# Kernel tuning notes

Hardware: AMD Instinct MI355X
Metric: run time of the kernel (lower is better)

The kernel has to match this reference:

```python
import jax, jax.numpy as jnp
import numpy as np
import math
from math import ceil

# --- static configuration (matches init_kwargs / input_specs) ---
T, H, W = 10, 45, 80            # native 720p latent video grid
NUM_WIN = (2, 5, 5)             # num_windows passed to make_720Pwindows_bysize
D_MODEL = 512
HEADS = 4
HEAD_DIM = 128
ROPE_DIMS = (32, 48, 48)        # 3D RoPE split of head_dim over (t, h, w)
THETA = 10000.0
TXT_LEN = 64
N_VID = T * H * W


def _make_windows():
    """Replicates make_720Pwindows_bysize slicing; returns gather/scatter index tables."""
    t, h, w = T, H, W
    rnt, rnh, rnw = NUM_WIN
    scale = math.sqrt(45 * 80 / (h * w))
    rh, rw = round(h * scale), round(w * scale)
    wh, ww = ceil(rh / rnh), ceil(rw / rnw)
    wt = ceil(min(t, 30) / rnt)
    nt, nh, nw = ceil(t / wt), ceil(h / wh), ceil(w / ww)
    lin = np.arange(t * h * w).reshape(t, h, w)
    wins = []
    for iw in range(nw):
        for ih in range(nh):
            for it in range(nt):
                ts = slice(it * wt, min((it + 1) * wt, t))
                hs = slice(ih * wh, min((ih + 1) * wh, h))
                ws = slice(iw * ww, min((iw + 1) * ww, w))
                blk = lin[ts, hs, ws].reshape(-1)
                if blk.size:
                    wins.append(blk)
    assert len({x.size for x in wins}) == 1, 'chosen dims give uniform windows'
    idx = np.stack(wins)                      # [n_win, win_size] gather index
    src = np.argsort(idx.reshape(-1))         # inverse permutation (un-window)
    return idx, src

WIN_IDX_NP, SRC_IDX_NP = _make_windows()
N_WIN, WIN_SIZE = WIN_IDX_NP.shape


def _rope_tables():
    """3D RoPE cos/sin per vid token: head_dim split over (t,h,w) axes, interleaved pairs."""
    tt = np.broadcast_to(np.arange(T)[:, None, None], (T, H, W)).reshape(-1)
    hh = np.broadcast_to(np.arange(H)[None, :, None], (T, H, W)).reshape(-1)
    ww = np.broadcast_to(np.arange(W)[None, None, :], (T, H, W)).reshape(-1)
    cos_l, sin_l = [], []
    for pos, d in zip((tt, hh, ww), ROPE_DIMS):
        inv = 1.0 / (THETA ** (np.arange(0, d, 2, dtype=np.float64) / d))
        ang = pos[:, None].astype(np.float64) * inv[None, :]
        ang = np.repeat(ang, 2, axis=-1)
        cos_l.append(np.cos(ang))
        sin_l.append(np.sin(ang))
    cos = np.concatenate(cos_l, -1).astype(np.float32)
    sin = np.concatenate(sin_l, -1).astype(np.float32)
    return jnp.asarray(cos), jnp.asarray(sin)  # each [N_VID, HEAD_DIM]

ROPE_COS, ROPE_SIN = _rope_tables()


def _rotate_half(x):
    # '... (d r) -> ... d r' with r=2, then (-x2, x1) re-interleaved
    xr = x.reshape(x.shape[:-1] + (-1, 2))
    x1, x2 = xr[..., 0], xr[..., 1]
    return jnp.stack((-x2, x1), axis=-1).reshape(x.shape)


def _apply_rope(x, cos, sin):
    # x: [N, heads, D]; cos/sin: [N, D]
    return x * cos[:, None, :] + _rotate_half(x) * sin[:, None, :]


def setup_inputs() -> dict:
    key = jax.random.key(0)
    ks = jax.random.split(key, 6)
    s = 1.0 / math.sqrt(D_MODEL)
    return {
        'vid': jax.random.normal(ks[0], (N_VID, D_MODEL), jnp.float32),
        'txt': jax.random.normal(ks[1], (TXT_LEN, D_MODEL), jnp.float32),
        'w_qkv_vid': jax.random.normal(ks[2], (D_MODEL, 3 * D_MODEL), jnp.float32) * s,
        'w_qkv_txt': jax.random.normal(ks[3], (D_MODEL, 3 * D_MODEL), jnp.float32) * s,
        'w_out_vid': jax.random.normal(ks[4], (D_MODEL, D_MODEL), jnp.float32) * s,
        'w_out_txt': jax.random.normal(ks[5], (D_MODEL, D_MODEL), jnp.float32) * s,
    }


def reference(vid, txt, w_qkv_vid, w_qkv_txt, w_out_vid, w_out_txt):
    win_idx = jnp.asarray(WIN_IDX_NP)
    src_idx = jnp.asarray(SRC_IDX_NP)
    # per-modality QKV projection (MMModule: separate vid/txt weights)
    qkv_v = (vid @ w_qkv_vid).reshape(N_VID, 3, HEADS, HEAD_DIM)
    qv, kv, vv = qkv_v[:, 0], qkv_v[:, 1], qkv_v[:, 2]
    qv = _apply_rope(qv, ROPE_COS, ROPE_SIN)   # 3D RoPE on video q/k only
    kv = _apply_rope(kv, ROPE_COS, ROPE_SIN)
    qkv_t = (txt @ w_qkv_txt).reshape(TXT_LEN, 3, HEADS, HEAD_DIM)
    qt, kt, vt = qkv_t[:, 0], qkv_t[:, 1], qkv_t[:, 2]

    def win_cat(xv, xt):
        xw = xv[win_idx]
        xtb = jnp.broadcast_to(xt[None], (N_WIN,) + xt.shape)    # txt repeated per window
        return jnp.concatenate([xw, xtb], axis=1)                # [n_win, S, H, D]

    q, k, v = win_cat(qv, qt), win_cat(kv, kt), win_cat(vv, vt)
    scale = 1.0 / math.sqrt(HEAD_DIM)
    scores = jnp.einsum('wqhd,wkhd->whqk', q, k) * scale         # [n_win, H, S, S]
    probs = jax.nn.softmax(scores, axis=-1)
    out = jnp.einsum('whqk,wkhd->wqhd', probs, v)                # [n_win, S, H, D]
    # un-window vid tokens (inverse permutation), mean-coalesce txt over windows
    out_v = out[:, :WIN_SIZE].reshape(N_WIN * WIN_SIZE, D_MODEL)[src_idx]
    out_t = out[:, WIN_SIZE:].mean(axis=0).reshape(TXT_LEN, D_MODEL)
    return jnp.concatenate([out_v @ w_out_vid, out_t @ w_out_txt], axis=0)
```

## Files before the change

kernel.cpp:

```cpp
#include <hip/hip_runtime.h>
#include <hip/hip_bf16.h>


typedef unsigned short u16;
typedef unsigned int   u32;
typedef float v4f __attribute__((ext_vector_type(4)));
typedef short v8s __attribute__((ext_vector_type(8)));

#define N_VID    36000
#define MPAD     36096
#define DM       512
#define NW       50
#define WSZ      720
#define SEQ      784
#define SP       832
#define QK_SCALE 0.08838834764831845f
#define L2THETA  13.287712379549449f

union U8 { uint4 u; u16 s[8]; };

__device__ __forceinline__ u16 f2b(float f) {
  u32 u = __builtin_bit_cast(u32, f);
  u32 r = (u + 0x7FFFu + ((u >> 16) & 1u)) >> 16;
  return (u16)r;
}
__device__ __forceinline__ float b2f(u16 h) {
  u32 u = ((u32)h) << 16;
  return __builtin_bit_cast(float, u);
}

__device__ __forceinline__ void gload_lds16(const void* g, void* l) {
  __builtin_amdgcn_global_load_lds(
      (const __attribute__((address_space(1))) void*)g,
      (__attribute__((address_space(3))) void*)l,
      16, 0, 0);
}

__global__ __launch_bounds__(256) void k_convert(const float* __restrict__ vid,
                                                 const float* __restrict__ txt,
                                                 u16* __restrict__ vid_b,
                                                 u16* __restrict__ txt_b) {
  int id  = blockIdx.x * 256 + threadIdx.x;
  int row = id >> 6, oct = id & 63;
  U8 o;
  if (row < MPAD) {
    if (row < N_VID) {
      const float* s = vid + (size_t)row * DM + oct * 8;
      float4 a = *(const float4*)s, b = *(const float4*)(s + 4);
      o.s[0]=f2b(a.x); o.s[1]=f2b(a.y); o.s[2]=f2b(a.z); o.s[3]=f2b(a.w);
      o.s[4]=f2b(b.x); o.s[5]=f2b(b.y); o.s[6]=f2b(b.z); o.s[7]=f2b(b.w);
    } else { o.u = make_uint4(0,0,0,0); }
    *(uint4*)&vid_b[(size_t)row * DM + oct * 8] = o.u;
  } else {
    int tr = row - MPAD;
    if (tr >= 128) return;
    if (tr < 64) {
      const float* s = txt + (size_t)tr * DM + oct * 8;
      float4 a = *(const float4*)s, b = *(const float4*)(s + 4);
      o.s[0]=f2b(a.x); o.s[1]=f2b(a.y); o.s[2]=f2b(a.z); o.s[3]=f2b(a.w);
      o.s[4]=f2b(b.x); o.s[5]=f2b(b.y); o.s[6]=f2b(b.z); o.s[7]=f2b(b.w);
    } else { o.u = make_uint4(0,0,0,0); }
    *(uint4*)&txt_b[(size_t)tr * DM + oct * 8] = o.u;
  }
}

__global__ __launch_bounds__(256) void k_transw(const float* __restrict__ wqv,
                                                const float* __restrict__ wqt,
                                                const float* __restrict__ wov,
                                                u16* __restrict__ o0,
                                                u16* __restrict__ o1,
                                                u16* __restrict__ o2) {
  __shared__ u16 lt[64 * 72];
  int b = blockIdx.x, t = threadIdx.x;
  const float* src; u16* dst; int N; int tb;
  if (b < 192)      { src = wqv; dst = o0; N = 1536; tb = b; }
  else if (b < 384) { src = wqt; dst = o1; N = 1536; tb = b - 192; }
  else              { src = wov; dst = o2; N = 512;  tb = b - 384; }
  int kt = tb & 7, nt = tb >> 3;
  int k0 = kt * 64, n0 = nt * 64;
#pragma unroll
  for (int pass = 0; pass < 16; ++pass) {
    int kl = pass * 4 + (t >> 6), nl = t & 63;
    float v = src[(size_t)(k0 + kl) * N + n0 + nl];
    lt[nl * 72 + kl] = f2b(v);
  }
  __syncthreads();
#pragma unroll
  for (int pass = 0; pass < 2; ++pass) {
    int slot = pass * 256 + t;
    int nr = slot >> 3, ko = slot & 7;
    U8 o;
#pragma unroll
    for (int j = 0; j < 8; ++j) o.s[j] = lt[nr * 72 + ko * 8 + j];
    *(uint4*)&dst[(size_t)(n0 + nr) * 512 + k0 + ko * 8] = o.u;
  }
}

template <int F32OUT>
__global__ __launch_bounds__(256) void k_gemm(const u16* __restrict__ A,
                                              const u16* __restrict__ Bt,
                                              void* __restrict__ Cout,
                                              int M, int N, int K, int Mstore) {
  __shared__ u16 lA[128 * 32];
  __shared__ u16 lB[128 * 32];
  int t = threadIdx.x, wv = t >> 6, L = t & 63;
  int m0 = blockIdx.x * 128, n0 = blockIdx.y * 128;
  int wm = wv & 1, wn = wv >> 1;
  v4f acc[4][4] = {};
  const int kiters = K >> 5;
  const u16* ga = A + (size_t)(m0 + wv * 32 + (L >> 2)) * K + (L & 3) * 8;
  const u16* gb = Bt + (size_t)(n0 + wv * 32 + (L >> 2)) * K + (L & 3) * 8;
  u16* la = lA + (wv * 32) * 32;
  u16* lb = lB + (wv * 32) * 32;
  for (int kt = 0; kt < kiters; ++kt) {
    __syncthreads();
    gload_lds16(ga,                 la);
    gload_lds16(ga + (size_t)16 * K, la + 16 * 32);
    gload_lds16(gb,                 lb);
    gload_lds16(gb + (size_t)16 * K, lb + 16 * 32);
    ga += 32; gb += 32;
    __syncthreads();
    v8s af[4], bf[4];
#pragma unroll
    for (int i = 0; i < 4; ++i) {
      af[i] = *(const v8s*)&lA[(wm * 64 + i * 16 + (L & 15)) * 32 + (L >> 4) * 8];
      bf[i] = *(const v8s*)&lB[(wn * 64 + i * 16 + (L & 15)) * 32 + (L >> 4) * 8];
    }
#pragma unroll
    for (int i = 0; i < 4; ++i)
#pragma unroll
      for (int j = 0; j < 4; ++j)
        acc[i][j] = __builtin_amdgcn_mfma_f32_16x16x32_bf16(af[i], bf[j], acc[i][j], 0, 0, 0);
  }
#pragma unroll
  for (int i = 0; i < 4; ++i) {
#pragma unroll
    for (int r = 0; r < 4; ++r) {
      int row = m0 + wm * 64 + i * 16 + (L >> 4) * 4 + r;
      if (row < Mstore) {
#pragma unroll
        for (int j = 0; j < 4; ++j) {
          int col = n0 + wn * 64 + j * 16 + (L & 15);
          if (F32OUT) ((float*)Cout)[(size_t)row * N + col] = acc[i][j][r];
          else        ((u16*)Cout)[(size_t)row * N + col] = f2b(acc[i][j][r]);
        }
      }
    }
  }
}

__global__ __launch_bounds__(256) void k_ropegather(const u16* __restrict__ qkv,
                                                    u16* __restrict__ Q,
                                                    u16* __restrict__ K,
                                                    u16* __restrict__ Vt) {
  __shared__ u16 lv[512 * 18];
  int t = threadIdx.x;
  int pt = blockIdx.x, w = blockIdx.y;
  int p_local = t >> 4;
  int p = pt * 16 + p_local;
  int iw = w / 10; int r10 = w - iw * 10; int ih = r10 >> 1; int it = r10 & 1;
  int dt = p / 144; int rem = p - dt * 144; int dh = rem >> 4; int dw = rem & 15;
  int tt = it * 5 + dt, hh = ih * 9 + dh, wx = iw * 16 + dw;
  int n = tt * 3600 + hh * 80 + wx;
  const size_t qrow = (size_t)n * 1536;
#pragma unroll
  for (int it2 = 0; it2 < 12; ++it2) {
    int oct = it2 * 16 + (t & 15);
    int col = oct * 8;
    U8 x; x.u = *(const uint4*)&qkv[qrow + col];
    if (col < 1024) {
      int cc = col & 511; int h = cc >> 7; int ch = cc & 127;
      int pos, i0; float dinv;
      if (ch < 32)      { pos = tt; i0 = ch >> 1;        dinv = 1.f / 32.f; }
      else if (ch < 80) { pos = hh; i0 = (ch - 32) >> 1; dinv = 1.f / 48.f; }
      else              { pos = wx; i0 = (ch - 80) >> 1; dinv = 1.f / 48.f; }
      bool isQ = col < 512;
      float sc = isQ ? QK_SCALE : 1.0f;
      U8 o;
#pragma unroll
      for (int pr = 0; pr < 4; ++pr) {
        float inv = exp2f(-2.f * (float)(i0 + pr) * dinv * L2THETA);
        float ang = (float)pos * inv;
        float s, c; __sincosf(ang, &s, &c);
        float x0 = b2f(x.s[2 * pr]), x1 = b2f(x.s[2 * pr + 1]);
        o.s[2 * pr]     = f2b((x0 * c - x1 * s) * sc);
        o.s[2 * pr + 1] = f2b((x1 * c + x0 * s) * sc);
      }
      u16* dst = isQ ? Q : K;
      *(uint4*)&dst[(((size_t)w * 4 + h) * SP + p) * 128 + ch] = o.u;
    } else {
      int cv = col - 1024;
#pragma unroll
      for (int j = 0; j < 8; ++j) lv[(cv + j) * 18 + p_local] = x.s[j];
    }
  }
  __syncthreads();
#pragma unroll
  for (int it3 = 0; it3 < 4; ++it3) {
    int slot = it3 * 256 + t; int cv = slot >> 1; int half = slot & 1;
    U8 o;
#pragma unroll
    for (int j = 0; j < 8; ++j) o.s[j] = lv[cv * 18 + half * 8 + j];
    int h = cv >> 7, ch = cv & 127;
    *(uint4*)&Vt[(((size_t)w * 4 + h) * 128 + ch) * SP + pt * 16 + half * 8] = o.u;
  }
}

__global__ __launch_bounds__(256) void k_txtfill(const u16* __restrict__ qkvt,
                                                 u16* __restrict__ Q,
                                                 u16* __restrict__ K,
                                                 u16* __restrict__ Vt) {
  int id = blockIdx.x * 256 + threadIdx.x;
  if (blockIdx.x < 800) {
    int c8 = id & 15, i = (id >> 4) & 63, wh = id >> 10;
    int h = wh & 3; int ch = c8 * 8;
    U8 q, k;
    q.u = *(const uint4*)&qkvt[(size_t)i * 1536 + h * 128 + ch];
    k.u = *(const uint4*)&qkvt[(size_t)i * 1536 + 512 + h * 128 + ch];
#pragma unroll
    for (int j = 0; j < 8; ++j) q.s[j] = f2b(b2f(q.s[j]) * QK_SCALE);
    int p = WSZ + i;
    size_t base = ((size_t)wh * SP + p) * 128 + ch;
    *(uint4*)&Q[base] = q.u;
    *(uint4*)&K[base] = k.u;
  } else {
    int id2 = id - 800 * 256;
    if (id2 >= 25600) return;
    int ch = id2 & 127; int wh = id2 >> 7; int h = wh & 3;
    u16 vals[64];
#pragma unroll
    for (int i = 0; i < 64; ++i)
      vals[i] = qkvt[(size_t)i * 1536 + 1024 + h * 128 + ch];
    size_t rb = ((size_t)wh * 128 + ch) * SP + WSZ;
#pragma unroll
    for (int j = 0; j < 8; ++j) {
      U8 o;
#pragma unroll
      for (int m = 0; m < 8; ++m) o.s[m] = vals[j * 8 + m];
      *(uint4*)&Vt[rb + j * 8] = o.u;
    }
  }
}

__global__ __launch_bounds__(256, 3) void k_attn(const u16* __restrict__ Q,
                                                 const u16* __restrict__ Kb,
                                                 const u16* __restrict__ Vt,
                                                 u16* __restrict__ outr,
                                                 float* __restrict__ txt_acc) {
  __shared__ u16 lK[4 * 64 * 32];
  __shared__ u16 lV[2 * 128 * 32];
  __shared__ u16 lP[4][32 * 72];
  int t = threadIdx.x, wv = t >> 6, L = t & 63;
  int qt = blockIdx.x, h = blockIdx.y, w = blockIdx.z;
  size_t whq = ((size_t)(w * 4 + h)) * SP * 128;
  int q0 = qt * 128 + wv * 32;
  if (q0 > 800) q0 = 800;
  int colL = L & 15;
  v8s qf[2][4];
#pragma unroll
  for (int s = 0; s < 2; ++s) {
    const u16* qp = Q + whq + (size_t)(q0 + s * 16 + colL) * 128 + (L >> 4) * 8;
#pragma unroll
    for (int kc = 0; kc < 4; ++kc) qf[s][kc] = *(const v8s*)(qp + kc * 32);
  }
  float li[2][4] = {};
  v4f O[2][8] = {};

  for (int kt = 0; kt < 13; ++kt) {
    __syncthreads();
#pragma unroll
    for (int pass = 0; pass < 4; ++pass) {
      int cr = wv * 64 + pass * 16 + (L >> 2);
      int kc = cr >> 6, row = cr & 63;
      gload_lds16(Kb + whq + (size_t)(kt * 64 + row) * 128 + kc * 32 + (L & 3) * 8,
                  (u16*)lK + (size_t)(wv * 64 + pass * 16) * 32);
      int kc2 = cr >> 7, ch = cr & 127;
      gload_lds16(Vt + whq + (size_t)ch * SP + kt * 64 + kc2 * 32 + (L & 3) * 8,
                  (u16*)lV + (size_t)(wv * 64 + pass * 16) * 32);
    }
    __syncthreads();

    v4f S[2][4] = {};
#pragma unroll
    for (int kc = 0; kc < 4; ++kc) {
#pragma unroll
      for (int nb = 0; nb < 4; ++nb) {
        v8s b = *(const v8s*)&lK[(kc * 64 + nb * 16 + colL) * 32 + (L >> 4) * 8];
        S[0][nb] = __builtin_amdgcn_mfma_f32_16x16x32_bf16(qf[0][kc], b, S[0][nb], 0, 0, 0);
        S[1][nb] = __builtin_amdgcn_mfma_f32_16x16x32_bf16(qf[1][kc], b, S[1][nb], 0, 0, 0);
      }
    }

#pragma unroll
    for (int s = 0; s < 2; ++s) {
#pragma unroll
      for (int nb = 0; nb < 4; ++nb) {
        bool valid = (kt * 64 + nb * 16 + colL) < SEQ;
#pragma unroll
        for (int r = 0; r < 4; ++r) {
          float e = valid ? __expf(S[s][nb][r]) : 0.f;
          li[s][r] += e;
          lP[wv][(s * 16 + (L >> 4) * 4 + r) * 72 + nb * 16 + colL] = f2b(e);
        }
      }
    }

#pragma unroll
    for (int kc2 = 0; kc2 < 2; ++kc2) {
      v8s pa0 = *(const v8s*)&lP[wv][(colL) * 72 + kc2 * 32 + (L >> 4) * 8];
      v8s pa1 = *(const v8s*)&lP[wv][(16 + colL) * 72 + kc2 * 32 + (L >> 4) * 8];
#pragma unroll
      for (int nbo = 0; nbo < 8; ++nbo) {
        v8s vb = *(const v8s*)&lV[(kc2 * 128 + nbo * 16 + colL) * 32 + (L >> 4) * 8];
        O[0][nbo] = __builtin_amdgcn_mfma_f32_16x16x32_bf16(pa0, vb, O[0][nbo], 0, 0, 0);
        O[1][nbo] = __builtin_amdgcn_mfma_f32_16x16x32_bf16(pa1, vb, O[1][nbo], 0, 0, 0);
      }
    }
  }

#pragma unroll
  for (int s = 0; s < 2; ++s)
#pragma unroll
    for (int r = 0; r < 4; ++r) {
      float v = li[s][r];
#pragma unroll
      for (int msk = 1; msk < 16; msk <<= 1) v += __shfl_xor(v, msk);
      li[s][r] = 1.f / v;
    }

  int iw = w / 10; int r10 = w - iw * 10; int ih = r10 >> 1; int it = r10 & 1;
#pragma unroll
  for (int s = 0; s < 2; ++s) {
#pragma unroll
    for (int r = 0; r < 4; ++r) {
      int p = q0 + s * 16 + (L >> 4) * 4 + r;
      float linv = li[s][r];
      if (p < WSZ) {
        int dt = p / 144; int rem = p - dt * 144; int dh = rem >> 4; int dw = rem & 15;
        int n = (it * 5 + dt) * 3600 + (ih * 9 + dh) * 80 + iw * 16 + dw;
        size_t rowbase = (size_t)n * DM + h * 128 + colL;
#pragma unroll
        for (int nbo = 0; nbo < 8; ++nbo)
          outr[rowbase + nbo * 16] = f2b(O[s][nbo][r] * linv);
      } else if (p < SEQ) {
        size_t rb = (size_t)(p - WSZ) * DM + h * 128 + colL;
#pragma unroll
        for (int nbo = 0; nbo < 8; ++nbo)
          atomicAdd(&txt_acc[rb + nbo * 16], O[s][nbo][r] * linv * 0.02f);
      }
    }
  }
}

__global__ __launch_bounds__(256) void k_txtout(const float* __restrict__ acc,
                                                const float* __restrict__ wo,
                                                float* __restrict__ ob) {
  int r = blockIdx.x, t = threadIdx.x;
  float s0 = 0.f, s1 = 0.f;
  for (int k = 0; k < 512; ++k) {
    float a = acc[r * 512 + k];
    s0 = fmaf(a, wo[k * 512 + t], s0);
    s1 = fmaf(a, wo[k * 512 + t + 256], s1);
  }
  ob[(size_t)r * 512 + t] = s0;
  ob[(size_t)r * 512 + t + 256] = s1;
}

extern "C" void kernel_launch(void* const* d_in, const int* in_sizes, int n_in,
                              void* d_out, int out_size, void* d_ws, size_t ws_size,
                              hipStream_t stream) {
  const float* vid       = (const float*)d_in[0];
  const float* txt       = (const float*)d_in[1];
  const float* w_qkv_vid = (const float*)d_in[2];
  const float* w_qkv_txt = (const float*)d_in[3];
  const float* w_out_vid = (const float*)d_in[4];
  const float* w_out_txt = (const float*)d_in[5];
  float* out = (float*)d_out;
  char* ws = (char*)d_ws;

  size_t off = 0;
  u16* vid_b   = (u16*)(ws + off); off += (size_t)MPAD * DM * 2;
  u16* txt_b   = (u16*)(ws + off); off += 128 * DM * 2;
  u16* wt_qv   = (u16*)(ws + off); off += 1536 * 512 * 2;
  u16* wt_qt   = (u16*)(ws + off); off += 1536 * 512 * 2;
  u16* wt_ov   = (u16*)(ws + off); off += 512 * 512 * 2;
  u16* qkv_v   = (u16*)(ws + off); off += (size_t)MPAD * 1536 * 2;
  u16* qkv_t   = (u16*)(ws + off); off += 128 * 1536 * 2;
  u16* Qb      = (u16*)(ws + off); off += (size_t)NW * 4 * SP * 128 * 2;
  u16* Kb      = (u16*)(ws + off); off += (size_t)NW * 4 * SP * 128 * 2;
  u16* Vtb     = (u16*)(ws + off); off += (size_t)NW * 4 * 128 * SP * 2;
  float* tacc  = (float*)(ws + off); off += 64 * 512 * 4;
  u16* out_rows = vid_b;

  hipMemsetAsync(tacc, 0, 64 * 512 * 4, stream);

  k_convert<<<9056, 256, 0, stream>>>(vid, txt, vid_b, txt_b);
  k_transw<<<448, 256, 0, stream>>>(w_qkv_vid, w_qkv_txt, w_out_vid, wt_qv, wt_qt, wt_ov);

  k_gemm<0><<<dim3(282, 12), 256, 0, stream>>>(vid_b, wt_qv, qkv_v, MPAD, 1536, 512, MPAD);
  k_gemm<0><<<dim3(1, 12), 256, 0, stream>>>(txt_b, wt_qt, qkv_t, 128, 1536, 512, 128);

  k_ropegather<<<dim3(45, 50), 256, 0, stream>>>(qkv_v, Qb, Kb, Vtb);
  k_txtfill<<<900, 256, 0, stream>>>(qkv_t, Qb, Kb, Vtb);

  k_attn<<<dim3(7, 4, 50), 256, 0, stream>>>(Qb, Kb, Vtb, out_rows, tacc);

  k_gemm<1><<<dim3(282, 4), 256, 0, stream>>>(out_rows, wt_ov, out, MPAD, 512, 512, N_VID);
  k_txtout<<<64, 256, 0, stream>>>(tacc, w_out_txt, out + (size_t)N_VID * DM);
}
```

Measured before the change: 517.2 us.

## Compute transposed scores so softmax probabilities feed PV MFMA from registers

The attention kernel now computes S^T = K·Q^T, which puts each query's probabilities in the MFMA register layout needed as the B operand of the PV product. The LDS round trip through the per-wave lP buffer is removed, and the row-sum reduction shrinks to two cross-lane shuffles. Blocks are remapped onto a 1D grid so that all query tiles of one window-head pair land on the same XCD, aiming for better L2 reuse of K and V. Output stores are widened to 8-byte packed writes, and the launch-bounds occupancy hint is dropped, which may change register allocation.

```diff
diff --git a/kernel.cpp b/kernel.cpp
--- a/kernel.cpp
+++ b/kernel.cpp
@@ -6,6 +6,7 @@
 typedef unsigned int   u32;
 typedef float v4f __attribute__((ext_vector_type(4)));
 typedef short v8s __attribute__((ext_vector_type(8)));
+typedef short v4s __attribute__((ext_vector_type(4)));
 
 #define N_VID    36000
 #define MPAD     36096
@@ -27,6 +28,10 @@
 __device__ __forceinline__ float b2f(u16 h) {
   u32 u = ((u32)h) << 16;
   return __builtin_bit_cast(float, u);
+}
+__device__ __forceinline__ u32 pkhi(float lo, float hi) {
+  return __builtin_amdgcn_perm(__builtin_bit_cast(u32, hi),
+                               __builtin_bit_cast(u32, lo), 0x07060302u);
 }
 
 __device__ __forceinline__ void gload_lds16(const void* g, void* l) {
@@ -242,28 +247,31 @@
   }
 }
 
-__global__ __launch_bounds__(256, 3) void k_attn(const u16* __restrict__ Q,
-                                                 const u16* __restrict__ Kb,
-                                                 const u16* __restrict__ Vt,
-                                                 u16* __restrict__ outr,
-                                                 float* __restrict__ txt_acc) {
+__global__ __launch_bounds__(256) void k_attn(const u16* __restrict__ Q,
+                                              const u16* __restrict__ Kb,
+                                              const u16* __restrict__ Vt,
+                                              u16* __restrict__ outr,
+                                              float* __restrict__ txt_acc) {
   __shared__ u16 lK[4 * 64 * 32];
   __shared__ u16 lV[2 * 128 * 32];
-  __shared__ u16 lP[4][32 * 72];
   int t = threadIdx.x, wv = t >> 6, L = t & 63;
-  int qt = blockIdx.x, h = blockIdx.y, w = blockIdx.z;
-  size_t whq = ((size_t)(w * 4 + h)) * SP * 128;
+  int id = blockIdx.x;
+  int xcd = id & 7, sidx = id >> 3;
+  int whg = sidx / 7;  int qt = sidx - whg * 7;
+  int wh = whg * 8 + xcd;
+  int w = wh >> 2, h = wh & 3;
+  size_t whq = ((size_t)wh) * SP * 128;
   int q0 = qt * 128 + wv * 32;
   if (q0 > 800) q0 = 800;
-  int colL = L & 15;
+  int colL = L & 15, quad = L >> 4;
   v8s qf[2][4];
 #pragma unroll
   for (int s = 0; s < 2; ++s) {
-    const u16* qp = Q + whq + (size_t)(q0 + s * 16 + colL) * 128 + (L >> 4) * 8;
+    const u16* qp = Q + whq + (size_t)(q0 + s * 16 + colL) * 128 + quad * 8;
 #pragma unroll
     for (int kc = 0; kc < 4; ++kc) qf[s][kc] = *(const v8s*)(qp + kc * 32);
   }
-  float li[2][4] = {};
+  float li[2] = {0.f, 0.f};
   v4f O[2][8] = {};
 
   for (int kt = 0; kt < 13; ++kt) {
@@ -280,74 +288,86 @@
     }
     __syncthreads();
 
-    v4f S[2][4] = {};
+    v4f ST[2][4] = {};
 #pragma unroll
     for (int kc = 0; kc < 4; ++kc) {
 #pragma unroll
-      for (int nb = 0; nb < 4; ++nb) {
-        v8s b = *(const v8s*)&lK[(kc * 64 + nb * 16 + colL) * 32 + (L >> 4) * 8];
-        S[0][nb] = __builtin_amdgcn_mfma_f32_16x16x32_bf16(qf[0][kc], b, S[0][nb], 0, 0, 0);
-        S[1][nb] = __builtin_amdgcn_mfma_f32_16x16x32_bf16(qf[1][kc], b, S[1][nb], 0, 0, 0);
-      }
-    }
-
+      for (int nbk = 0; nbk < 4; ++nbk) {
+        v8s kf = *(const v8s*)&lK[(kc * 64 + nbk * 16 + colL) * 32 + quad * 8];
+        ST[0][nbk] = __builtin_amdgcn_mfma_f32_16x16x32_bf16(kf, qf[0][kc], ST[0][nbk], 0, 0, 0);
+        ST[1][nbk] = __builtin_amdgcn_mfma_f32_16x16x32_bf16(kf, qf[1][kc], ST[1][nbk], 0, 0, 0);
+      }
+    }
+
+    union { v8s v; u32 wd[4]; } Bf[2][2];
 #pragma unroll
     for (int s = 0; s < 2; ++s) {
 #pragma unroll
-      for (int nb = 0; nb < 4; ++nb) {
-        bool valid = (kt * 64 + nb * 16 + colL) < SEQ;
-#pragma unroll
-        for (int r = 0; r < 4; ++r) {
-          float e = valid ? __expf(S[s][nb][r]) : 0.f;
-          li[s][r] += e;
-          lP[wv][(s * 16 + (L >> 4) * 4 + r) * 72 + nb * 16 + colL] = f2b(e);
+      for (int nbk = 0; nbk < 4; ++nbk) {
+        float ev[4];
+        if (kt * 64 + nbk * 16 < SEQ) {
+#pragma unroll
+          for (int r = 0; r < 4; ++r) {
+            float e = __expf(ST[s][nbk][r]);
+            u32 tb = __builtin_bit_cast(u32, e) & 0xFFFF0000u;
+            float tf = __builtin_bit_cast(float, tb);
+            li[s] += tf;
+            ev[r] = tf;
+          }
+        } else {
+#pragma unroll
+          for (int r = 0; r < 4; ++r) ev[r] = 0.f;
         }
+        Bf[nbk >> 1][s].wd[(nbk & 1) * 2 + 0] = pkhi(ev[0], ev[1]);
+        Bf[nbk >> 1][s].wd[(nbk & 1) * 2 + 1] = pkhi(ev[2], ev[3]);
       }
     }
 
 #pragma unroll
     for (int kc2 = 0; kc2 < 2; ++kc2) {
-      v8s pa0 = *(const v8s*)&lP[wv][(colL) * 72 + kc2 * 32 + (L >> 4) * 8];
-      v8s pa1 = *(const v8s*)&lP[wv][(16 + colL) * 72 + kc2 * 32 + (L >> 4) * 8];
 #pragma unroll
       for (int nbo = 0; nbo < 8; ++nbo) {
-        v8s vb = *(const v8s*)&lV[(kc2 * 128 + nbo * 16 + colL) * 32 + (L >> 4) * 8];
-        O[0][nbo] = __builtin_amdgcn_mfma_f32_16x16x32_bf16(pa0, vb, O[0][nbo], 0, 0, 0);
-        O[1][nbo] = __builtin_amdgcn_mfma_f32_16x16x32_bf16(pa1, vb, O[1][nbo], 0, 0, 0);
-      }
-    }
-  }
-
-#pragma unroll
-  for (int s = 0; s < 2; ++s)
-#pragma unroll
-    for (int r = 0; r < 4; ++r) {
-      float v = li[s][r];
-#pragma unroll
-      for (int msk = 1; msk < 16; msk <<= 1) v += __shfl_xor(v, msk);
-      li[s][r] = 1.f / v;
-    }
+        const u16* vp = &lV[(kc2 * 128 + nbo * 16 + colL) * 32 + quad * 4];
+        v4s lo = *(const v4s*)vp;
+        v4s hi = *(const v4s*)(vp + 16);
+        v8s af = __builtin_shufflevector(lo, hi, 0, 1, 2, 3, 4, 5, 6, 7);
+        O[0][nbo] = __builtin_amdgcn_mfma_f32_16x16x32_bf16(af, Bf[kc2][0].v, O[0][nbo], 0, 0, 0);
+        O[1][nbo] = __builtin_amdgcn_mfma_f32_16x16x32_bf16(af, Bf[kc2][1].v, O[1][nbo], 0, 0, 0);
+      }
+    }
+  }
+
+  float linv[2];
+#pragma unroll
+  for (int s = 0; s < 2; ++s) {
+    float v = li[s];
+    v += __shfl_xor(v, 16);
+    v += __shfl_xor(v, 32);
+    linv[s] = 1.f / v;
+  }
 
   int iw = w / 10; int r10 = w - iw * 10; int ih = r10 >> 1; int it = r10 & 1;
 #pragma unroll
   for (int s = 0; s < 2; ++s) {
-#pragma unroll
-    for (int r = 0; r < 4; ++r) {
-      int p = q0 + s * 16 + (L >> 4) * 4 + r;
-      float linv = li[s][r];
-      if (p < WSZ) {
-        int dt = p / 144; int rem = p - dt * 144; int dh = rem >> 4; int dw = rem & 15;
-        int n = (it * 5 + dt) * 3600 + (ih * 9 + dh) * 80 + iw * 16 + dw;
-        size_t rowbase = (size_t)n * DM + h * 128 + colL;
-#pragma unroll
-        for (int nbo = 0; nbo < 8; ++nbo)
-          outr[rowbase + nbo * 16] = f2b(O[s][nbo][r] * linv);
-      } else if (p < SEQ) {
-        size_t rb = (size_t)(p - WSZ) * DM + h * 128 + colL;
-#pragma unroll
-        for (int nbo = 0; nbo < 8; ++nbo)
-          atomicAdd(&txt_acc[rb + nbo * 16], O[s][nbo][r] * linv * 0.02f);
-      }
+    int p = q0 + s * 16 + colL;
+    if (p < WSZ) {
+      int dt = p / 144; int rem = p - dt * 144; int dh = rem >> 4; int dw = rem & 15;
+      int n = (it * 5 + dt) * 3600 + (ih * 9 + dh) * 80 + iw * 16 + dw;
+      size_t rowbase = (size_t)n * DM + h * 128 + quad * 4;
+#pragma unroll
+      for (int nbo = 0; nbo < 8; ++nbo) {
+        uint2 st;
+        st.x = (u32)f2b(O[s][nbo][0] * linv[s]) | ((u32)f2b(O[s][nbo][1] * linv[s]) << 16);
+        st.y = (u32)f2b(O[s][nbo][2] * linv[s]) | ((u32)f2b(O[s][nbo][3] * linv[s]) << 16);
+        *(uint2*)&outr[rowbase + nbo * 16] = st;
+      }
+    } else if (p < SEQ) {
+      size_t rb = (size_t)(p - WSZ) * DM + h * 128 + quad * 4;
+#pragma unroll
+      for (int nbo = 0; nbo < 8; ++nbo)
+#pragma unroll
+        for (int r = 0; r < 4; ++r)
+          atomicAdd(&txt_acc[rb + nbo * 16 + r], O[s][nbo][r] * linv[s] * 0.02f);
     }
   }
 }
@@ -403,7 +423,7 @@
   k_ropegather<<<dim3(45, 50), 256, 0, stream>>>(qkv_v, Qb, Kb, Vtb);
   k_txtfill<<<900, 256, 0, stream>>>(qkv_t, Qb, Kb, Vtb);
 
-  k_attn<<<dim3(7, 4, 50), 256, 0, stream>>>(Qb, Kb, Vtb, out_rows, tacc);
+  k_attn<<<1400, 256, 0, stream>>>(Qb, Kb, Vtb, out_rows, tacc);
 
   k_gemm<1><<<dim3(282, 4), 256, 0, stream>>>(out_rows, wt_ov, out, MPAD, 512, 512, N_VID);
   k_txtout<<<64, 256, 0, stream>>>(tacc, w_out_txt, out + (size_t)N_VID * DM);
```

Result: slower. 579.6 us (+12.1%).
